# Optimization experiments

Measured on AMD Instinct MI355X. Metric: run time of the kernel, lower is better.

Reference implementation:

```python
import jax, jax.numpy as jnp
import numpy as np

H = 1024      # hidden_size
I = 2048      # intermediate_size
E = 32        # num_routed_experts
B, S = 4, 2048


def setup_inputs() -> dict:
    key = jax.random.key(0)
    ks = jax.random.split(key, 8)
    scale = 0.02
    inp = {
        "hidden_states": jax.random.normal(ks[0], (B, S, H), dtype=jnp.float32),
        # router gate: stored [H, E] so logits = x @ gate_w
        "gate_w": jax.random.normal(ks[1], (H, E), dtype=jnp.float32) * scale,
        # shared SwiGLU (num_shared_experts=1), weights stored [in, out]
        "shared_gate_w": jax.random.normal(ks[2], (H, I), dtype=jnp.float32) * scale,
        "shared_up_w": jax.random.normal(ks[3], (H, I), dtype=jnp.float32) * scale,
        "shared_down_w": jax.random.normal(ks[4], (I, H), dtype=jnp.float32) * scale,
        # routed grouped SwiGLU, weights stored [E, in, out] (matches GroupedLinear)
        "routed_gate_w": jax.random.normal(ks[5], (E, H, I), dtype=jnp.float32) * scale,
        "routed_up_w": jax.random.normal(ks[6], (E, H, I), dtype=jnp.float32) * scale,
        "routed_down_w": jax.random.normal(ks[7], (E, I, H), dtype=jnp.float32) * scale,
    }
    return inp


def _grouped_mm(a, w, group_sizes):
    # a: [T, in], w: [E, in, out], group_sizes: [E] int32 -> [T, out]
    return jax.lax.ragged_dot(a, w, group_sizes)


def _swiglu(x, gw, uw, dw):
    return (jax.nn.silu(x @ gw) * (x @ uw)) @ dw


def reference(hidden_states, gate_w, shared_gate_w, shared_up_w, shared_down_w,
              routed_gate_w, routed_up_w, routed_down_w):
    b, s, h = hidden_states.shape
    x = hidden_states.reshape(-1, h)                      # [T, H]

    # ---- shared expert ----
    shared_out = _swiglu(x, shared_gate_w, shared_up_w, shared_down_w)

    # ---- router: top-1 ----
    logits = x @ gate_w                                   # [T, E]
    topk_ids = jnp.argmax(logits, axis=-1)                # [T]
    topk_val = jnp.max(logits, axis=-1)                   # [T]
    scores = jax.nn.sigmoid(topk_val)[:, None]            # [T, 1]
    xs = x * scores                                       # scale tokens by router score

    # ---- dispatch: sort tokens by expert id ----
    tokens_per_expert = jnp.zeros((E,), jnp.int32).at[topk_ids].add(1)
    order = jnp.argsort(topk_ids)                         # token ids sorted by expert
    sorted_x = xs[order]                                  # [T, H]

    # ---- grouped SwiGLU experts ----
    g = _grouped_mm(sorted_x, routed_gate_w, tokens_per_expert)   # [T, I]
    u = _grouped_mm(sorted_x, routed_up_w, tokens_per_expert)     # [T, I]
    d = _grouped_mm(jax.nn.silu(g) * u, routed_down_w, tokens_per_expert)  # [T, H]

    # ---- combine: unsort back to token order ----
    inv = jnp.argsort(order)
    routed_out = d[inv]

    return (shared_out + routed_out).reshape(b, s, h)
```

## Files before the change

kernel.cpp:

```cpp
#include <hip/hip_runtime.h>
#include <stdint.h>
#include <stddef.h>

#define TOK 8192
#define H 1024
#define IDIM 2048
#define NE 32
#define BM 128
#define BN 64
#define BK 64
#define MAX_TILES 96

typedef __attribute__((ext_vector_type(8))) short short8;
typedef __attribute__((ext_vector_type(4))) float f32x4;
typedef __attribute__((ext_vector_type(4))) float float4v;
typedef __attribute__((ext_vector_type(2))) unsigned int uint2v;
typedef __attribute__((ext_vector_type(4))) unsigned int uint4v;


__device__ __forceinline__ unsigned short f2bf(float x) {
  unsigned u = __builtin_bit_cast(unsigned, x);
  u += 0x7fffu + ((u >> 16) & 1u);
  return (unsigned short)(u >> 16);
}

__device__ __forceinline__ unsigned cvtpk(float lo, float hi) {
  unsigned r;
  asm("v_cvt_pk_bf16_f32 %0, %1, %2" : "=v"(r) : "v"(lo), "v"(hi));
  return r;
}

__device__ __forceinline__ void gll16(const void* g, void* l) {
  __builtin_amdgcn_global_load_lds(
      (const __attribute__((address_space(1))) unsigned int*)g,
      (__attribute__((address_space(3))) unsigned int*)l, 16, 0, 0);
}

__device__ __forceinline__ f32x4 mfma16(short8 a, short8 b, f32x4 c) {
  return __builtin_amdgcn_mfma_f32_16x16x32_bf16(a, b, c, 0, 0, 0);
}

__device__ __forceinline__ int wswz(int n) {
  return ((n ^ (n >> 2)) & 7) << 4;
}


__global__ __launch_bounds__(256) void router_kernel(
    const float* __restrict__ x, const float* __restrict__ gw,
    unsigned short* __restrict__ xbf, unsigned short* __restrict__ xsbf,
    int* __restrict__ expert_id, int* __restrict__ counts)
{
  __shared__ float xl[8 * H];
  __shared__ float plog[8][8][NE];
  __shared__ float sscore[8];
  const int tid = threadIdx.x;
  const long t0 = (long)blockIdx.x * 8;

  const float4v* src = (const float4v*)(x + t0 * H);
  float4v* dst = (float4v*)xl;
  #pragma unroll
  for (int i = 0; i < 8; ++i) dst[tid + i * 256] = src[tid + i * 256];
  __syncthreads();

  {
    const int e = tid & 31, c = tid >> 5;
    float acc[8] = {0, 0, 0, 0, 0, 0, 0, 0};
    const float* gp = gw + (c * 128) * NE + e;
    for (int h = 0; h < 128; ++h) {
      float g = gp[h * NE];
      const float* xr = xl + (c * 128 + h);
      #pragma unroll
      for (int tk = 0; tk < 8; ++tk) acc[tk] += xr[tk * H] * g;
    }
    #pragma unroll
    for (int tk = 0; tk < 8; ++tk) plog[c][tk][e] = acc[tk];
  }
  __syncthreads();
  {
    const int e = tid & 31, tok = tid >> 5;
    float lg = 0.f;
    #pragma unroll
    for (int c = 0; c < 8; ++c) lg += plog[c][tok][e];
    float m = lg; int be = e;
    #pragma unroll
    for (int mask = 16; mask >= 1; mask >>= 1) {
      float om = __shfl_xor(m, mask);
      int   oe = __shfl_xor(be, mask);
      if (om > m || (om == m && oe < be)) { m = om; be = oe; }
    }
    if (e == 0) {
      sscore[tok] = 1.f / (1.f + __expf(-m));
      expert_id[t0 + tok] = be;
      atomicAdd(&counts[be], 1);
    }
  }
  __syncthreads();
  {
    const float sc = sscore[tid >> 5];
    const int base = (tid >> 5) * H + (tid & 31) * 32;
    #pragma unroll
    for (int i = 0; i < 4; ++i) {
      uint4v vx, vs;
      #pragma unroll
      for (int q = 0; q < 4; ++q) {
        const float a = xl[base + i * 8 + 2 * q];
        const float b = xl[base + i * 8 + 2 * q + 1];
        vx[q] = cvtpk(a, b);
        vs[q] = cvtpk(a * sc, b * sc);
      }
      *(uint4v*)(xbf  + t0 * H + base + i * 8) = vx;
      *(uint4v*)(xsbf + t0 * H + base + i * 8) = vs;
    }
  }
}


__global__ void scan_kernel(const int* __restrict__ counts, int* __restrict__ offsets,
                            int* __restrict__ cursor, int* __restrict__ tile_e,
                            int* __restrict__ tile_p, int* __restrict__ n_tiles)
{
  if (threadIdx.x != 0) return;
  int off = 0, nt = 0;
  for (int e = 0; e < NE; ++e) {
    offsets[e] = off; cursor[e] = off;
    int cc = counts[e];
    for (int k = 0; k < cc; k += BM) { tile_e[nt] = e; tile_p[nt] = off + k; ++nt; }
    off += cc;
  }
  offsets[NE] = off;
  n_tiles[0] = nt;
}


__global__ __launch_bounds__(256) void perm_kernel(
    const int* __restrict__ expert_id, int* __restrict__ cursor, int* __restrict__ perm)
{
  int t = blockIdx.x * 256 + threadIdx.x;
  int e = expert_id[t];
  int pos = atomicAdd(&cursor[e], 1);
  perm[pos] = t;
}


template<bool ROUTED>
__global__ __launch_bounds__(256, 3) void gateup_kernel(
    const unsigned short* __restrict__ Abase,
    const float* __restrict__ WgAll, const float* __restrict__ WuAll,
    unsigned short* __restrict__ act,
    const int* __restrict__ perm, const int* __restrict__ tile_e,
    const int* __restrict__ tile_p, const int* __restrict__ offsets,
    const int* __restrict__ n_tiles)
{
  __shared__ short Alds[2][BM * BK];
  __shared__ short Glds[BN * BK];
  __shared__ short Ulds[BN * BK];

  const int tid = threadIdx.x;
  const int wave = tid >> 6, lane = tid & 63;

  int row0, row_end;
  const float *Wg, *Wu;
  if constexpr (ROUTED) {
    if ((int)blockIdx.x >= *n_tiles) return;
    const int e = tile_e[blockIdx.x];
    row0 = tile_p[blockIdx.x];
    row_end = offsets[e + 1];
    Wg = WgAll + (size_t)e * H * IDIM;
    Wu = WuAll + (size_t)e * H * IDIM;
  } else {
    row0 = blockIdx.x * BM; row_end = row0 + BM;
    Wg = WgAll; Wu = WuAll;
  }
  const int n0 = blockIdx.y * BN;

  const unsigned short* asrc[4];
  int aoff[4];
  #pragma unroll
  for (int i = 0; i < 4; ++i) {
    const int r = wave * 32 + i * 8 + (lane >> 3);
    int grow;
    if constexpr (ROUTED) {
      int p = row0 + r;
      if (p >= row_end) p = row0;
      grow = perm[p];
    } else grow = row0 + r;
    const int cb = ((lane & 7) * 16) ^ ((r & 7) << 4);
    asrc[i] = Abase + (size_t)grow * H + (cb >> 1);
    aoff[i] = (wave * 32 + i * 8) * BK;
  }

  const int wq = tid >> 4;
  const int wc = tid & 15;

  f32x4 accg[2][4] = {};
  f32x4 accu[2][4] = {};
  float4v g4[4], u4[4];

  auto stageA = [&](int kt) {
    short* base = Alds[kt & 1];
    #pragma unroll
    for (int i = 0; i < 4; ++i) gll16(asrc[i] + kt * BK, base + aoff[i]);
  };
  auto loadW = [&](int kt) {
    const int k0 = kt * BK;
    #pragma unroll
    for (int r = 0; r < 4; ++r) {
      const size_t goff = (size_t)(k0 + wq * 4 + r) * IDIM + (n0 + wc * 4);
      g4[r] = *(const float4v*)(Wg + goff);
      u4[r] = *(const float4v*)(Wu + goff);
    }
  };
  auto writeW = [&]() {
    #pragma unroll
    for (int j = 0; j < 4; ++j) {
      const int n = wc * 4 + j;
      const int cb = (wq * 8) ^ wswz(n);
      uint2v pg, pu;
      pg.x = cvtpk(g4[0][j], g4[1][j]);
      pg.y = cvtpk(g4[2][j], g4[3][j]);
      pu.x = cvtpk(u4[0][j], u4[1][j]);
      pu.y = cvtpk(u4[2][j], u4[3][j]);
      *(uint2v*)((char*)Glds + n * 128 + cb) = pg;
      *(uint2v*)((char*)Ulds + n * 128 + cb) = pu;
    }
  };
  auto compute = [&](int kt) {
    const char* ab = (const char*)Alds[kt & 1];
    #pragma unroll
    for (int kk = 0; kk < 2; ++kk) {
      short8 af[2];
      #pragma unroll
      for (int m = 0; m < 2; ++m) {
        const int r = wave * 32 + m * 16 + (lane & 15);
        const int cb = (kk * 64 + ((lane >> 4) * 16)) ^ ((r & 7) << 4);
        af[m] = *(const short8*)(ab + r * 128 + cb);
      }
      #pragma unroll
      for (int nf = 0; nf < 4; ++nf) {
        const int n = nf * 16 + (lane & 15);
        const int cb = (kk * 64 + ((lane >> 4) * 16)) ^ wswz(n);
        short8 bg = *(const short8*)((const char*)Glds + n * 128 + cb);
        short8 bu = *(const short8*)((const char*)Ulds + n * 128 + cb);
        #pragma unroll
        for (int m = 0; m < 2; ++m) {
          accg[m][nf] = mfma16(af[m], bg, accg[m][nf]);
          accu[m][nf] = mfma16(af[m], bu, accu[m][nf]);
        }
      }
    }
  };

  stageA(0);
  loadW(0);
  writeW();
  __syncthreads();

  #pragma unroll 1
  for (int kt = 0; kt < H / BK - 1; ++kt) {
    stageA(kt + 1);
    loadW(kt + 1);
    compute(kt);
    __syncthreads();
    writeW();
    __syncthreads();
  }
  compute(H / BK - 1);

  #pragma unroll
  for (int m = 0; m < 2; ++m)
    #pragma unroll
    for (int nf = 0; nf < 4; ++nf) {
      const int col = n0 + nf * 16 + (lane & 15);
      #pragma unroll
      for (int j = 0; j < 4; ++j) {
        const int row = row0 + wave * 32 + m * 16 + ((lane >> 4) * 4) + j;
        if (ROUTED && row >= row_end) continue;
        const float g = accg[m][nf][j];
        const float u = accu[m][nf][j];
        const float v = (g / (1.f + __expf(-g))) * u;
        act[(size_t)row * IDIM + col] = f2bf(v);
      }
    }
}


template<bool ROUTED>
__global__ __launch_bounds__(256, 4) void down_kernel(
    const unsigned short* __restrict__ act,
    const float* __restrict__ WdAll,
    float* __restrict__ out,
    const int* __restrict__ perm, const int* __restrict__ tile_e,
    const int* __restrict__ tile_p, const int* __restrict__ offsets,
    const int* __restrict__ n_tiles)
{
  __shared__ short Alds[2][BM * BK];
  __shared__ short Wlds[BN * BK];

  const int tid = threadIdx.x;
  const int wave = tid >> 6, lane = tid & 63;

  int row0, row_end;
  const float* Wd;
  if constexpr (ROUTED) {
    if ((int)blockIdx.x >= *n_tiles) return;
    const int e = tile_e[blockIdx.x];
    row0 = tile_p[blockIdx.x];
    row_end = offsets[e + 1];
    Wd = WdAll + (size_t)e * IDIM * H;
  } else {
    row0 = blockIdx.x * BM; row_end = row0 + BM;
    Wd = WdAll;
  }
  const int n0 = blockIdx.y * BN;

  const unsigned short* asrc[4];
  int aoff[4];
  #pragma unroll
  for (int i = 0; i < 4; ++i) {
    const int r = wave * 32 + i * 8 + (lane >> 3);
    int p = row0 + r;
    if (ROUTED && p >= row_end) p = row0;
    const int cb = ((lane & 7) * 16) ^ ((r & 7) << 4);
    asrc[i] = act + (size_t)p * IDIM + (cb >> 1);
    aoff[i] = (wave * 32 + i * 8) * BK;
  }

  const int wq = tid >> 4;
  const int wc = tid & 15;

  f32x4 acc[2][4] = {};
  float4v w4[4];

  auto stageA = [&](int kt) {
    short* base = Alds[kt & 1];
    #pragma unroll
    for (int i = 0; i < 4; ++i) gll16(asrc[i] + kt * BK, base + aoff[i]);
  };
  auto loadW = [&](int kt) {
    const int k0 = kt * BK;
    #pragma unroll
    for (int r = 0; r < 4; ++r)
      w4[r] = *(const float4v*)(Wd + (size_t)(k0 + wq * 4 + r) * H + (n0 + wc * 4));
  };
  auto writeW = [&]() {
    #pragma unroll
    for (int j = 0; j < 4; ++j) {
      const int n = wc * 4 + j;
      const int cb = (wq * 8) ^ wswz(n);
      uint2v pw;
      pw.x = cvtpk(w4[0][j], w4[1][j]);
      pw.y = cvtpk(w4[2][j], w4[3][j]);
      *(uint2v*)((char*)Wlds + n * 128 + cb) = pw;
    }
  };
  auto compute = [&](int kt) {
    const char* ab = (const char*)Alds[kt & 1];
    #pragma unroll
    for (int kk = 0; kk < 2; ++kk) {
      short8 af[2];
      #pragma unroll
      for (int m = 0; m < 2; ++m) {
        const int r = wave * 32 + m * 16 + (lane & 15);
        const int cb = (kk * 64 + ((lane >> 4) * 16)) ^ ((r & 7) << 4);
        af[m] = *(const short8*)(ab + r * 128 + cb);
      }
      #pragma unroll
      for (int nf = 0; nf < 4; ++nf) {
        const int n = nf * 16 + (lane & 15);
        const int cb = (kk * 64 + ((lane >> 4) * 16)) ^ wswz(n);
        short8 bw = *(const short8*)((const char*)Wlds + n * 128 + cb);
        #pragma unroll
        for (int m = 0; m < 2; ++m) acc[m][nf] = mfma16(af[m], bw, acc[m][nf]);
      }
    }
  };

  stageA(0);
  loadW(0);
  writeW();
  __syncthreads();

  #pragma unroll 1
  for (int kt = 0; kt < IDIM / BK - 1; ++kt) {
    stageA(kt + 1);
    loadW(kt + 1);
    compute(kt);
    __syncthreads();
    writeW();
    __syncthreads();
  }
  compute(IDIM / BK - 1);

  #pragma unroll
  for (int m = 0; m < 2; ++m)
    #pragma unroll
    for (int nf = 0; nf < 4; ++nf) {
      const int col = n0 + nf * 16 + (lane & 15);
      #pragma unroll
      for (int j = 0; j < 4; ++j) {
        const int row = row0 + wave * 32 + m * 16 + ((lane >> 4) * 4) + j;
        const float v = acc[m][nf][j];
        if constexpr (ROUTED) {
          if (row < row_end) {
            const int t = perm[row];
            out[(size_t)t * H + col] += v;
          }
        } else {
          out[(size_t)row * H + col] = v;
        }
      }
    }
}


extern "C" void kernel_launch(void* const* d_in, const int* in_sizes, int n_in,
                              void* d_out, int out_size, void* d_ws, size_t ws_size,
                              hipStream_t stream) {
  (void)in_sizes; (void)n_in; (void)out_size; (void)ws_size;
  const float* x      = (const float*)d_in[0];
  const float* gate_w = (const float*)d_in[1];
  const float* sgw    = (const float*)d_in[2];
  const float* suw    = (const float*)d_in[3];
  const float* sdw    = (const float*)d_in[4];
  const float* rgw    = (const float*)d_in[5];
  const float* ruw    = (const float*)d_in[6];
  const float* rdw    = (const float*)d_in[7];
  float* out = (float*)d_out;

  char* ws = (char*)d_ws;
  unsigned short* xbf  = (unsigned short*)(ws + 0);
  unsigned short* xsbf = (unsigned short*)(ws + 16777216);
  unsigned short* act  = (unsigned short*)(ws + 33554432);
  int* perm      = (int*)(ws + 67108864);
  int* expert_id = (int*)(ws + 67141632);
  int* counts    = (int*)(ws + 67174400);
  int* offsets   = (int*)(ws + 67174528);
  int* cursor    = (int*)(ws + 67174784);
  int* tile_e    = (int*)(ws + 67174912);
  int* tile_p    = (int*)(ws + 67175424);
  int* n_tiles   = (int*)(ws + 67175936);

  hipMemsetAsync(counts, 0, NE * sizeof(int), stream);
  router_kernel<<<TOK / 8, 256, 0, stream>>>(x, gate_w, xbf, xsbf, expert_id, counts);
  scan_kernel<<<1, 64, 0, stream>>>(counts, offsets, cursor, tile_e, tile_p, n_tiles);
  perm_kernel<<<TOK / 256, 256, 0, stream>>>(expert_id, cursor, perm);

  gateup_kernel<false><<<dim3(TOK / BM, IDIM / BN), 256, 0, stream>>>(
      xbf, sgw, suw, act, perm, tile_e, tile_p, offsets, n_tiles);
  down_kernel<false><<<dim3(TOK / BM, H / BN), 256, 0, stream>>>(
      act, sdw, out, perm, tile_e, tile_p, offsets, n_tiles);
  gateup_kernel<true><<<dim3(MAX_TILES, IDIM / BN), 256, 0, stream>>>(
      xsbf, rgw, ruw, act, perm, tile_e, tile_p, offsets, n_tiles);
  down_kernel<true><<<dim3(MAX_TILES, H / BN), 256, 0, stream>>>(
      act, rdw, out, perm, tile_e, tile_p, offsets, n_tiles);
}
```

Baseline: 661.0 us.

## Split fused gate/up GEMM into separate up and gate passes via unified template

Replaces the fused gate+up kernel, which computed both projections per tile, with a single templated GEMM run twice. The up pass writes bf16 results to the activation buffer. The gate pass reads them back and applies SiLU-times-up in its epilogue. This lowers per-block register and LDS use so occupancy can rise (launch bounds 4 instead of 3), but it re-reads the A tiles, adds a bf16 write and read round trip of the intermediate, and rounds u to bf16 before the multiply.

```diff
diff --git a/kernel.cpp b/kernel.cpp
--- a/kernel.cpp
+++ b/kernel.cpp
@@ -22,6 +22,11 @@
   unsigned u = __builtin_bit_cast(unsigned, x);
   u += 0x7fffu + ((u >> 16) & 1u);
   return (unsigned short)(u >> 16);
+}
+
+__device__ __forceinline__ float bf2f(unsigned short h) {
+  unsigned u = ((unsigned)h) << 16;
+  return __builtin_bit_cast(float, u);
 }
 
 __device__ __forceinline__ unsigned cvtpk(float lo, float hi) {
@@ -142,153 +147,12 @@
 }
 
 
-template<bool ROUTED>
-__global__ __launch_bounds__(256, 3) void gateup_kernel(
-    const unsigned short* __restrict__ Abase,
-    const float* __restrict__ WgAll, const float* __restrict__ WuAll,
-    unsigned short* __restrict__ act,
-    const int* __restrict__ perm, const int* __restrict__ tile_e,
-    const int* __restrict__ tile_p, const int* __restrict__ offsets,
-    const int* __restrict__ n_tiles)
-{
-  __shared__ short Alds[2][BM * BK];
-  __shared__ short Glds[BN * BK];
-  __shared__ short Ulds[BN * BK];
-
-  const int tid = threadIdx.x;
-  const int wave = tid >> 6, lane = tid & 63;
-
-  int row0, row_end;
-  const float *Wg, *Wu;
-  if constexpr (ROUTED) {
-    if ((int)blockIdx.x >= *n_tiles) return;
-    const int e = tile_e[blockIdx.x];
-    row0 = tile_p[blockIdx.x];
-    row_end = offsets[e + 1];
-    Wg = WgAll + (size_t)e * H * IDIM;
-    Wu = WuAll + (size_t)e * H * IDIM;
-  } else {
-    row0 = blockIdx.x * BM; row_end = row0 + BM;
-    Wg = WgAll; Wu = WuAll;
-  }
-  const int n0 = blockIdx.y * BN;
-
-  const unsigned short* asrc[4];
-  int aoff[4];
-  #pragma unroll
-  for (int i = 0; i < 4; ++i) {
-    const int r = wave * 32 + i * 8 + (lane >> 3);
-    int grow;
-    if constexpr (ROUTED) {
-      int p = row0 + r;
-      if (p >= row_end) p = row0;
-      grow = perm[p];
-    } else grow = row0 + r;
-    const int cb = ((lane & 7) * 16) ^ ((r & 7) << 4);
-    asrc[i] = Abase + (size_t)grow * H + (cb >> 1);
-    aoff[i] = (wave * 32 + i * 8) * BK;
-  }
-
-  const int wq = tid >> 4;
-  const int wc = tid & 15;
-
-  f32x4 accg[2][4] = {};
-  f32x4 accu[2][4] = {};
-  float4v g4[4], u4[4];
-
-  auto stageA = [&](int kt) {
-    short* base = Alds[kt & 1];
-    #pragma unroll
-    for (int i = 0; i < 4; ++i) gll16(asrc[i] + kt * BK, base + aoff[i]);
-  };
-  auto loadW = [&](int kt) {
-    const int k0 = kt * BK;
-    #pragma unroll
-    for (int r = 0; r < 4; ++r) {
-      const size_t goff = (size_t)(k0 + wq * 4 + r) * IDIM + (n0 + wc * 4);
-      g4[r] = *(const float4v*)(Wg + goff);
-      u4[r] = *(const float4v*)(Wu + goff);
-    }
-  };
-  auto writeW = [&]() {
-    #pragma unroll
-    for (int j = 0; j < 4; ++j) {
-      const int n = wc * 4 + j;
-      const int cb = (wq * 8) ^ wswz(n);
-      uint2v pg, pu;
-      pg.x = cvtpk(g4[0][j], g4[1][j]);
-      pg.y = cvtpk(g4[2][j], g4[3][j]);
-      pu.x = cvtpk(u4[0][j], u4[1][j]);
-      pu.y = cvtpk(u4[2][j], u4[3][j]);
-      *(uint2v*)((char*)Glds + n * 128 + cb) = pg;
-      *(uint2v*)((char*)Ulds + n * 128 + cb) = pu;
-    }
-  };
-  auto compute = [&](int kt) {
-    const char* ab = (const char*)Alds[kt & 1];
-    #pragma unroll
-    for (int kk = 0; kk < 2; ++kk) {
-      short8 af[2];
-      #pragma unroll
-      for (int m = 0; m < 2; ++m) {
-        const int r = wave * 32 + m * 16 + (lane & 15);
-        const int cb = (kk * 64 + ((lane >> 4) * 16)) ^ ((r & 7) << 4);
-        af[m] = *(const short8*)(ab + r * 128 + cb);
-      }
-      #pragma unroll
-      for (int nf = 0; nf < 4; ++nf) {
-        const int n = nf * 16 + (lane & 15);
-        const int cb = (kk * 64 + ((lane >> 4) * 16)) ^ wswz(n);
-        short8 bg = *(const short8*)((const char*)Glds + n * 128 + cb);
-        short8 bu = *(const short8*)((const char*)Ulds + n * 128 + cb);
-        #pragma unroll
-        for (int m = 0; m < 2; ++m) {
-          accg[m][nf] = mfma16(af[m], bg, accg[m][nf]);
-          accu[m][nf] = mfma16(af[m], bu, accu[m][nf]);
-        }
-      }
-    }
-  };
-
-  stageA(0);
-  loadW(0);
-  writeW();
-  __syncthreads();
-
-  #pragma unroll 1
-  for (int kt = 0; kt < H / BK - 1; ++kt) {
-    stageA(kt + 1);
-    loadW(kt + 1);
-    compute(kt);
-    __syncthreads();
-    writeW();
-    __syncthreads();
-  }
-  compute(H / BK - 1);
-
-  #pragma unroll
-  for (int m = 0; m < 2; ++m)
-    #pragma unroll
-    for (int nf = 0; nf < 4; ++nf) {
-      const int col = n0 + nf * 16 + (lane & 15);
-      #pragma unroll
-      for (int j = 0; j < 4; ++j) {
-        const int row = row0 + wave * 32 + m * 16 + ((lane >> 4) * 4) + j;
-        if (ROUTED && row >= row_end) continue;
-        const float g = accg[m][nf][j];
-        const float u = accu[m][nf][j];
-        const float v = (g / (1.f + __expf(-g))) * u;
-        act[(size_t)row * IDIM + col] = f2bf(v);
-      }
-    }
-}
-
-
-template<bool ROUTED>
-__global__ __launch_bounds__(256, 4) void down_kernel(
-    const unsigned short* __restrict__ act,
-    const float* __restrict__ WdAll,
-    float* __restrict__ out,
+template<bool ROUTED, bool APERM, int KD, int ND, int EPI>
+__global__ __launch_bounds__(256, 4) void gemm_kernel(
+    const unsigned short* __restrict__ A,
+    const float* __restrict__ Wall,
+    float* __restrict__ outf,
+    unsigned short* __restrict__ outh,
     const int* __restrict__ perm, const int* __restrict__ tile_e,
     const int* __restrict__ tile_p, const int* __restrict__ offsets,
     const int* __restrict__ n_tiles)
@@ -300,16 +164,16 @@
   const int wave = tid >> 6, lane = tid & 63;
 
   int row0, row_end;
-  const float* Wd;
+  const float* W;
   if constexpr (ROUTED) {
     if ((int)blockIdx.x >= *n_tiles) return;
     const int e = tile_e[blockIdx.x];
     row0 = tile_p[blockIdx.x];
     row_end = offsets[e + 1];
-    Wd = WdAll + (size_t)e * IDIM * H;
+    W = Wall + (size_t)e * KD * ND;
   } else {
     row0 = blockIdx.x * BM; row_end = row0 + BM;
-    Wd = WdAll;
+    W = Wall;
   }
   const int n0 = blockIdx.y * BN;
 
@@ -320,8 +184,10 @@
     const int r = wave * 32 + i * 8 + (lane >> 3);
     int p = row0 + r;
     if (ROUTED && p >= row_end) p = row0;
+    int grow = p;
+    if constexpr (ROUTED && APERM) grow = perm[p];
     const int cb = ((lane & 7) * 16) ^ ((r & 7) << 4);
-    asrc[i] = act + (size_t)p * IDIM + (cb >> 1);
+    asrc[i] = A + (size_t)grow * KD + (cb >> 1);
     aoff[i] = (wave * 32 + i * 8) * BK;
   }
 
@@ -340,7 +206,7 @@
     const int k0 = kt * BK;
     #pragma unroll
     for (int r = 0; r < 4; ++r)
-      w4[r] = *(const float4v*)(Wd + (size_t)(k0 + wq * 4 + r) * H + (n0 + wc * 4));
+      w4[r] = *(const float4v*)(W + (size_t)(k0 + wq * 4 + r) * ND + (n0 + wc * 4));
   };
   auto writeW = [&]() {
     #pragma unroll
@@ -381,7 +247,7 @@
   __syncthreads();
 
   #pragma unroll 1
-  for (int kt = 0; kt < IDIM / BK - 1; ++kt) {
+  for (int kt = 0; kt < KD / BK - 1; ++kt) {
     stageA(kt + 1);
     loadW(kt + 1);
     compute(kt);
@@ -389,7 +255,7 @@
     writeW();
     __syncthreads();
   }
-  compute(IDIM / BK - 1);
+  compute(KD / BK - 1);
 
   #pragma unroll
   for (int m = 0; m < 2; ++m)
@@ -399,14 +265,19 @@
       #pragma unroll
       for (int j = 0; j < 4; ++j) {
         const int row = row0 + wave * 32 + m * 16 + ((lane >> 4) * 4) + j;
+        if (ROUTED && row >= row_end) continue;
         const float v = acc[m][nf][j];
-        if constexpr (ROUTED) {
-          if (row < row_end) {
-            const int t = perm[row];
-            out[(size_t)t * H + col] += v;
-          }
+        if constexpr (EPI == 0) {
+          outh[(size_t)row * ND + col] = f2bf(v);
+        } else if constexpr (EPI == 1) {
+          const float u = bf2f(outh[(size_t)row * ND + col]);
+          const float s = v / (1.f + __expf(-v));
+          outh[(size_t)row * ND + col] = f2bf(s * u);
+        } else if constexpr (EPI == 2) {
+          outf[(size_t)row * ND + col] = v;
         } else {
-          out[(size_t)row * H + col] = v;
+          const int t = perm[row];
+          outf[(size_t)t * ND + col] += v;
         }
       }
     }
@@ -445,12 +316,17 @@
   scan_kernel<<<1, 64, 0, stream>>>(counts, offsets, cursor, tile_e, tile_p, n_tiles);
   perm_kernel<<<TOK / 256, 256, 0, stream>>>(expert_id, cursor, perm);
 
-  gateup_kernel<false><<<dim3(TOK / BM, IDIM / BN), 256, 0, stream>>>(
-      xbf, sgw, suw, act, perm, tile_e, tile_p, offsets, n_tiles);
-  down_kernel<false><<<dim3(TOK / BM, H / BN), 256, 0, stream>>>(
-      act, sdw, out, perm, tile_e, tile_p, offsets, n_tiles);
-  gateup_kernel<true><<<dim3(MAX_TILES, IDIM / BN), 256, 0, stream>>>(
-      xsbf, rgw, ruw, act, perm, tile_e, tile_p, offsets, n_tiles);
-  down_kernel<true><<<dim3(MAX_TILES, H / BN), 256, 0, stream>>>(
-      act, rdw, out, perm, tile_e, tile_p, offsets, n_tiles);
-}
+  gemm_kernel<false, false, H, IDIM, 0><<<dim3(TOK / BM, IDIM / BN), 256, 0, stream>>>(
+      xbf, suw, nullptr, act, perm, tile_e, tile_p, offsets, n_tiles);
+  gemm_kernel<false, false, H, IDIM, 1><<<dim3(TOK / BM, IDIM / BN), 256, 0, stream>>>(
+      xbf, sgw, nullptr, act, perm, tile_e, tile_p, offsets, n_tiles);
+  gemm_kernel<false, false, IDIM, H, 2><<<dim3(TOK / BM, H / BN), 256, 0, stream>>>(
+      act, sdw, out, nullptr, perm, tile_e, tile_p, offsets, n_tiles);
+
+  gemm_kernel<true, true, H, IDIM, 0><<<dim3(MAX_TILES, IDIM / BN), 256, 0, stream>>>(
+      xsbf, ruw, nullptr, act, perm, tile_e, tile_p, offsets, n_tiles);
+  gemm_kernel<true, true, H, IDIM, 1><<<dim3(MAX_TILES, IDIM / BN), 256, 0, stream>>>(
+      xsbf, rgw, nullptr, act, perm, tile_e, tile_p, offsets, n_tiles);
+  gemm_kernel<true, false, IDIM, H, 3><<<dim3(MAX_TILES, H / BN), 256, 0, stream>>>(
+      act, rdw, out, nullptr, perm, tile_e, tile_p, offsets, n_tiles);
+}
```

After: 742.6 us. 12.3% more time.
